# Performance work log

Hardware: AMD Instinct MI355X
Metric: run time of the kernel (lower is better)

Reference implementation:

```python
import jax, jax.numpy as jnp
import numpy as np


def setup_inputs() -> dict:
    key = jax.random.key(0)
    k1, k2 = jax.random.split(key)
    B, C, H, W = 2, 32, 128, 240
    left_feature = jax.random.normal(k1, (B, C, H, W), dtype=jnp.float32)
    right_feature = jax.random.normal(k2, (B, C, H, W), dtype=jnp.float32)
    return {"left_feature": left_feature, "right_feature": right_feature, "max_disp": 192}


def reference(left_feature, right_feature, max_disp):
    # Faithful vectorized version of the shifted-slice-copy cost volume:
    #   cv[:, :C, d, :, w] = left[:, :, :, w]        if w >= d else 0
    #   cv[:, C:, d, :, w] = right[:, :, :, w - d]   if w >= d else 0
    B, C, H, W = left_feature.shape
    D = max_disp // 4
    d = jnp.arange(D)[:, None]          # [D, 1]
    w = jnp.arange(W)[None, :]          # [1, W]
    mask = (w >= d)                     # [D, W] valid region per disparity
    mask_b = mask[None, None, :, None, :]  # [1,1,D,1,W]

    # Left half: same slice broadcast over all disparities, zero where w < d.
    left_vol = jnp.where(mask_b, left_feature[:, :, None, :, :], jnp.float32(0))

    # Right half: gather column w-d (clipped; masked to zero where invalid).
    idx = jnp.clip(w - d, 0, W - 1)                      # [D, W]
    right_g = jnp.take(right_feature, idx, axis=3)       # [B, C, H, D, W]
    right_vol = jnp.where(mask_b, jnp.moveaxis(right_g, 3, 2), jnp.float32(0))

    return jnp.concatenate([left_vol, right_vol], axis=1)  # [B, 2C, D, H, W]
```

## Files before the change

kernel.cpp:

```cpp
#include <hip/hip_runtime.h>

constexpr int B  = 2;
constexpr int C  = 32;
constexpr int H  = 128;
constexpr int W  = 240;
constexpr int D  = 48;
constexpr int C2 = 2 * C;
constexpr int W4 = W / 4;
constexpr int DSTRIDE = H * W4;
constexpr int NT = B * C2 * H * W4;

typedef float nfloat4 __attribute__((ext_vector_type(4)));

__device__ __forceinline__ void nt_store(float4* p, float x, float y, float z, float w)
{
    nfloat4 v = { x, y, z, w };
    __builtin_nontemporal_store(v, reinterpret_cast<nfloat4*>(p));
}

__global__ __launch_bounds__(256)
void cost_volume_kernel(const float* __restrict__ left,
                        const float* __restrict__ right,
                        float4* __restrict__ out)
{
    int v = blockIdx.x * blockDim.x + threadIdx.x;
    if (v >= NT) return;

    int w4 = v % W4;
    int t  = v / W4;
    int h  = t % H;  t /= H;
    int c2 = t % C2;
    int b  = t / C2;
    int w0 = w4 * 4;

    float4* outp = out + ((b * C2 + c2) * D * H + h) * W4 + w4;

    if (c2 < C) {
        const float* src = left + ((b * C + c2) * H + h) * W;
        float4 vv = *reinterpret_cast<const float4*>(src + w0);
#pragma unroll
        for (int d = 0; d < D; ++d) {
            nt_store(outp + d * DSTRIDE,
                     (w0 + 0 >= d) ? vv.x : 0.0f,
                     (w0 + 1 >= d) ? vv.y : 0.0f,
                     (w0 + 2 >= d) ? vv.z : 0.0f,
                     (w0 + 3 >= d) ? vv.w : 0.0f);
        }
    } else {
        const float* srow = right + ((b * C + (c2 - C)) * H + h) * W;
        float4 A = *reinterpret_cast<const float4*>(srow + w0);
#pragma unroll
        for (int g = 0; g < D / 4; ++g) {
            int qb = w4 - g - 1;
            int qbc = qb < 0 ? 0 : qb;
            float4 Bq = *reinterpret_cast<const float4*>(srow + 4 * qbc);
            float win[8] = { Bq.x, Bq.y, Bq.z, Bq.w, A.x, A.y, A.z, A.w };
#pragma unroll
            for (int s = 0; s < 4; ++s) {
                const int d = 4 * g + s;
                nt_store(outp + d * DSTRIDE,
                         (w0 + 0 >= d) ? win[4 + 0 - s] : 0.0f,
                         (w0 + 1 >= d) ? win[4 + 1 - s] : 0.0f,
                         (w0 + 2 >= d) ? win[4 + 2 - s] : 0.0f,
                         (w0 + 3 >= d) ? win[4 + 3 - s] : 0.0f);
            }
            A = Bq;
        }
    }
}

extern "C" void kernel_launch(void* const* d_in, const int* in_sizes, int n_in,
                              void* d_out, int out_size, void* d_ws, size_t ws_size,
                              hipStream_t stream)
{
    const float* left  = (const float*)d_in[0];
    const float* right = (const float*)d_in[1];
    float4* out = (float4*)d_out;

    constexpr int BLOCK = 256;
    constexpr int GRID  = (NT + BLOCK - 1) / BLOCK;
    cost_volume_kernel<<<GRID, BLOCK, 0, stream>>>(left, right, out);
}
```

Baseline: 143.3 us.

## Restructure cost volume so each block writes contiguous 4-disparity slabs from LDS tile

Each block now owns one (batch, channel, 4-disparity group, half-height) slab. It stages the 64-row input tile into shared memory, then writes four fully contiguous output planes. Before, each thread wrote 48 strided float4 stores across disparity planes. The goal is more sequential write streams per block and a large grid for better write coalescing and DRAM locality. The cost is that input is re-read once per disparity group (12x input traffic, mostly L2 hits), plus 61KB of LDS per block, which limits occupancy.

```diff
diff --git a/kernel.cpp b/kernel.cpp
--- a/kernel.cpp
+++ b/kernel.cpp
@@ -7,8 +7,13 @@
 constexpr int D  = 48;
 constexpr int C2 = 2 * C;
 constexpr int W4 = W / 4;
-constexpr int DSTRIDE = H * W4;
-constexpr int NT = B * C2 * H * W4;
+constexpr int QPS = H * W4;
+constexpr int HROWS = 64;
+constexpr int QPB = HROWS * W4;
+constexpr int BLOCK = 256;
+constexpr int KS = QPB / BLOCK;
+constexpr int NDQ = D / 4;
+constexpr int GRID = B * C2 * NDQ * 2;
 
 typedef float nfloat4 __attribute__((ext_vector_type(4)));
 
@@ -23,48 +28,67 @@
                         const float* __restrict__ right,
                         float4* __restrict__ out)
 {
-    int v = blockIdx.x * blockDim.x + threadIdx.x;
-    if (v >= NT) return;
+    __shared__ float4 lds[QPB];
 
-    int w4 = v % W4;
-    int t  = v / W4;
-    int h  = t % H;  t /= H;
-    int c2 = t % C2;
-    int b  = t / C2;
-    int w0 = w4 * 4;
+    int bid   = blockIdx.x;
+    int rh    = bid & 1;
+    int t     = bid >> 1;
+    int dq    = t % NDQ;
+    int plane = t / NDQ;
+    int c2    = plane & (C2 - 1);
+    int b     = plane >> 6;
 
-    float4* outp = out + ((b * C2 + c2) * D * H + h) * W4 + w4;
+    const float* baseimg = (c2 < C)
+        ? left  + (size_t)((b * C + c2)       * H) * W
+        : right + (size_t)((b * C + (c2 - C)) * H) * W;
+    const float4* img = reinterpret_cast<const float4*>(baseimg + rh * HROWS * W);
+#pragma unroll
+    for (int k = 0; k < KS; ++k) {
+        int qi = (int)threadIdx.x + k * BLOCK;
+        lds[qi] = img[qi];
+    }
+    __syncthreads();
+
+    float4* outbase = out + ((size_t)plane * D + 4 * dq) * QPS + rh * QPB;
 
     if (c2 < C) {
-        const float* src = left + ((b * C + c2) * H + h) * W;
-        float4 vv = *reinterpret_cast<const float4*>(src + w0);
 #pragma unroll
-        for (int d = 0; d < D; ++d) {
-            nt_store(outp + d * DSTRIDE,
-                     (w0 + 0 >= d) ? vv.x : 0.0f,
-                     (w0 + 1 >= d) ? vv.y : 0.0f,
-                     (w0 + 2 >= d) ? vv.z : 0.0f,
-                     (w0 + 3 >= d) ? vv.w : 0.0f);
+        for (int k = 0; k < KS; ++k) {
+            int qi  = (int)threadIdx.x + k * BLOCK;
+            int row = qi / W4;
+            int w4  = qi - row * W4;
+            int m   = w4 * 4 - 4 * dq;
+            float4 v = lds[qi];
+#pragma unroll
+            for (int dd = 0; dd < 4; ++dd) {
+                nt_store(outbase + dd * QPS + qi,
+                         (m + 0 >= dd) ? v.x : 0.0f,
+                         (m + 1 >= dd) ? v.y : 0.0f,
+                         (m + 2 >= dd) ? v.z : 0.0f,
+                         (m + 3 >= dd) ? v.w : 0.0f);
+            }
         }
     } else {
-        const float* srow = right + ((b * C + (c2 - C)) * H + h) * W;
-        float4 A = *reinterpret_cast<const float4*>(srow + w0);
 #pragma unroll
-        for (int g = 0; g < D / 4; ++g) {
-            int qb = w4 - g - 1;
-            int qbc = qb < 0 ? 0 : qb;
-            float4 Bq = *reinterpret_cast<const float4*>(srow + 4 * qbc);
-            float win[8] = { Bq.x, Bq.y, Bq.z, Bq.w, A.x, A.y, A.z, A.w };
+        for (int k = 0; k < KS; ++k) {
+            int qi  = (int)threadIdx.x + k * BLOCK;
+            int row = qi / W4;
+            int w4  = qi - row * W4;
+            int m   = (w4 - dq) * 4;
+            int hq  = w4 - dq;
+            int lq  = hq - 1;
+            int rowbase = row * W4;
+            float4 Hi = lds[rowbase + (hq < 0 ? 0 : hq)];
+            float4 Lo = lds[rowbase + (lq < 0 ? 0 : lq)];
+            float win[8] = { Lo.x, Lo.y, Lo.z, Lo.w, Hi.x, Hi.y, Hi.z, Hi.w };
 #pragma unroll
-            for (int s = 0; s < 4; ++s) {
-                const int d = 4 * g + s;
-                nt_store(outp + d * DSTRIDE,
-                         (w0 + 0 >= d) ? win[4 + 0 - s] : 0.0f,
-                         (w0 + 1 >= d) ? win[4 + 1 - s] : 0.0f,
-                         (w0 + 2 >= d) ? win[4 + 2 - s] : 0.0f,
-                         (w0 + 3 >= d) ? win[4 + 3 - s] : 0.0f);
+            for (int dd = 0; dd < 4; ++dd) {
+                nt_store(outbase + dd * QPS + qi,
+                         (m + 0 >= dd) ? win[4 + 0 - dd] : 0.0f,
+                         (m + 1 >= dd) ? win[4 + 1 - dd] : 0.0f,
+                         (m + 2 >= dd) ? win[4 + 2 - dd] : 0.0f,
+                         (m + 3 >= dd) ? win[4 + 3 - dd] : 0.0f);
             }
-            A = Bq;
         }
     }
 }
@@ -77,7 +101,5 @@
     const float* right = (const float*)d_in[1];
     float4* out = (float4*)d_out;
 
-    constexpr int BLOCK = 256;
-    constexpr int GRID  = (NT + BLOCK - 1) / BLOCK;
     cost_volume_kernel<<<GRID, BLOCK, 0, stream>>>(left, right, out);
 }
```

New measurement: 149.7 us. +4.5%, slower.
